# Performance work log

Measured on AMD Instinct MI355X. Metric: run time of the kernel, lower is better.

The kernel has to match this reference:

```python
import jax, jax.numpy as jnp
import numpy as np

N_NODES = 100000
N_EDGES = 1600000
D_IN = 64
D_OUT = 64


def setup_inputs() -> dict:
    key = jax.random.key(0)
    k1, k2, k3, k4, k5 = jax.random.split(key, 5)
    features = jax.random.normal(k1, (N_NODES, D_IN), dtype=jnp.float32)
    edge_row = jax.random.randint(k2, (N_EDGES,), 0, N_NODES, dtype=jnp.int32)
    edge_col = jax.random.randint(k3, (N_EDGES,), 0, N_NODES, dtype=jnp.int32)
    edge_val = jax.random.uniform(k4, (N_EDGES,), dtype=jnp.float32)
    # learned parameters (xavier-uniform kernel, zero bias, ones skip weight)
    limit = float(np.sqrt(6.0 / (D_IN + D_OUT)))
    kernel = jax.random.uniform(k5, (D_IN, D_OUT), minval=-limit, maxval=limit, dtype=jnp.float32)
    bias = jnp.zeros((D_OUT,), dtype=jnp.float32)
    skip_weight = jnp.ones((D_OUT,), dtype=jnp.float32)
    return {
        "features": features,
        "kernel": kernel,
        "bias": bias,
        "skip_weight": skip_weight,
        "edge_row": edge_row,
        "edge_col": edge_col,
        "edge_val": edge_val,
    }


def reference(features, kernel, bias, skip_weight, edge_row, edge_col, edge_val):
    # dense projection: [n, d_in] @ [d_in, d_out]
    h = features @ kernel
    # SpMM: (A h)[r] = sum_{edges e with row r} val_e * h[col_e]
    gathered = h[edge_col] * edge_val[:, None]  # [n_edges, d_out]
    agg = jax.ops.segment_sum(gathered, edge_row, num_segments=N_NODES)
    out = h * skip_weight + agg + bias
    return jax.nn.selu(out)
```

## Files before the change

kernel.cpp:

```cpp
#include <hip/hip_runtime.h>
#include <math.h>

#define N_NODES 100000
#define N_EDGES 1600000
#define D 64
#define RPB 128
#define NBUK 782
#define CAP 3072
#define NGB 782
#define NHB 196
#define EPB 8192
#define POFF_STRIDE 200

typedef unsigned int u32;
typedef unsigned short u16;

static __device__ __forceinline__ u32 f2bf(float x) {
    u32 u = __float_as_uint(x);
    u32 r = u + 0x7FFFu + ((u >> 16) & 1u);
    return r >> 16;
}
static __device__ __forceinline__ u32 pack2(float a, float b) {
    return f2bf(a) | (f2bf(b) << 16);
}
static __device__ __forceinline__ float bflo(u32 u) { return __uint_as_float(u << 16); }
static __device__ __forceinline__ float bfhi(u32 u) { return __uint_as_float(u & 0xFFFF0000u); }
static __device__ __forceinline__ float selu(float x) {
    const float scale = 1.0507009873554805f;
    const float alpha = 1.6732632423543772f;
    return x > 0.f ? scale * x : scale * alpha * (expf(x) - 1.f);
}

__global__ __launch_bounds__(256) void fused_gemm_sort(
    const float* __restrict__ feat, const float* __restrict__ kern,
    const int* __restrict__ erow, const int* __restrict__ ecol,
    const float* __restrict__ eval, u16* __restrict__ hbf,
    int2* __restrict__ sedge, u32* __restrict__ poff)
{
    __shared__ u32 smem[10795];
    const int t = threadIdx.x;

    if (blockIdx.x < NGB) {
        float* ks = (float*)smem;
        {
            const float4* k4 = (const float4*)kern;
            float4* ks4 = (float4*)ks;
            #pragma unroll
            for (int i = 0; i < 4; i++) ks4[t + 256 * i] = k4[t + 256 * i];
        }
        __syncthreads();

        const int cgi  = t & 7;
        const int rg   = t >> 3;
        const int row0 = blockIdx.x * RPB + rg * 4;

        float4 acc[4][2];
        #pragma unroll
        for (int r = 0; r < 4; r++)
            #pragma unroll
            for (int i = 0; i < 2; i++)
                acc[r][i] = make_float4(0.f, 0.f, 0.f, 0.f);

        #pragma unroll 4
        for (int s = 0; s < 16; s++) {
            float4 f[4];
            #pragma unroll
            for (int r = 0; r < 4; r++) {
                int row = min(row0 + r, N_NODES - 1);
                f[r] = ((const float4*)(feat + (size_t)row * D))[s];
            }
            float4 kk[4][2];
            #pragma unroll
            for (int kv = 0; kv < 4; kv++)
                #pragma unroll
                for (int i = 0; i < 2; i++)
                    kk[kv][i] = ((const float4*)(ks + (s * 4 + kv) * D))[cgi * 2 + i];
            #pragma unroll
            for (int r = 0; r < 4; r++) {
                #pragma unroll
                for (int kv = 0; kv < 4; kv++) {
                    float fv = (&f[r].x)[kv];
                    #pragma unroll
                    for (int i = 0; i < 2; i++) {
                        acc[r][i].x += fv * kk[kv][i].x;
                        acc[r][i].y += fv * kk[kv][i].y;
                        acc[r][i].z += fv * kk[kv][i].z;
                        acc[r][i].w += fv * kk[kv][i].w;
                    }
                }
            }
        }

        #pragma unroll
        for (int r = 0; r < 4; r++) {
            int row = row0 + r;
            if (row < N_NODES) {
                uint4 o;
                o.x = pack2(acc[r][0].x, acc[r][0].y);
                o.y = pack2(acc[r][0].z, acc[r][0].w);
                o.z = pack2(acc[r][1].x, acc[r][1].y);
                o.w = pack2(acc[r][1].z, acc[r][1].w);
                ((uint4*)(hbf + (size_t)row * D))[cgi] = o;
            }
        }
    } else {
        u32* er   = smem;
        u32* c    = smem + 8192;
        u32* o    = c + NBUK;
        u32* cu   = o + NBUK + 1;
        u32* part = cu + NBUK;

        for (int i = t; i < NBUK; i += 256) c[i] = 0u;
        __syncthreads();

        const int hb   = blockIdx.x - NGB;
        const int base = hb * EPB;

        #pragma unroll
        for (int k = 0; k < 32; k++) {
            int i = base + k * 256 + t;
            u32 r = 0xFFFFFFFFu;
            if (i < N_EDGES) { r = (u32)erow[i]; atomicAdd(&c[r >> 7], 1u); }
            er[k * 256 + t] = r;
        }
        __syncthreads();

        const int i0 = t * 4;
        {
            u32 p = 0u;
            #pragma unroll
            for (int j = 0; j < 4; j++) { int i = i0 + j; if (i < NBUK) p += c[i]; }
            part[t] = p;
        }
        __syncthreads();
        for (int d = 1; d < 256; d <<= 1) {
            u32 a = (t >= d) ? part[t - d] : 0u;
            __syncthreads();
            part[t] += a;
            __syncthreads();
        }
        {
            u32 run = (t > 0) ? part[t - 1] : 0u;
            #pragma unroll
            for (int j = 0; j < 4; j++) {
                int i = i0 + j;
                if (i < NBUK) { o[i] = run; cu[i] = run; run += c[i]; }
            }
            if (t == 255) o[NBUK] = part[255];
        }
        __syncthreads();

        #pragma unroll
        for (int k = 0; k < 32; k++) {
            int i = base + k * 256 + t;
            if (i < N_EDGES) {
                u32 r = er[k * 256 + t];
                u32 rk = atomicAdd(&cu[r >> 7], 1u);
                sedge[(size_t)hb * EPB + rk] =
                    make_int2(ecol[i] | (int)((r & 127u) << 17),
                              __float_as_int(eval[i]));
            }
        }

        for (int i = t; i <= NBUK; i += 256)
            poff[(size_t)i * POFF_STRIDE + hb] = o[i];
    }
}

__global__ __launch_bounds__(1024) void agg_kernel(
    const u32* __restrict__ poff, const int2* __restrict__ sedge,
    const u16* __restrict__ hbf, const float* __restrict__ skip,
    const float* __restrict__ bias, float* __restrict__ out)
{
    __shared__ int2 eB[CAP];
    __shared__ u32 c[RPB];
    __shared__ u32 o[RPB];
    __shared__ u32 cur[RPB];
    __shared__ u32 rs0[NHB];
    __shared__ u32 rlen[NHB];

    const int t = threadIdx.x;
    const int w = t >> 6;
    const int lane = t & 63;
    const int b = blockIdx.x;

    if (t < RPB) c[t] = 0u;
    if (t < NHB) {
        u32 s0 = poff[(size_t)b * POFF_STRIDE + t];
        u32 s1 = poff[(size_t)(b + 1) * POFF_STRIDE + t];
        rs0[t]  = s0;
        rlen[t] = s1 - s0;
    }
    __syncthreads();

    for (int hb = w; hb < NHB; hb += 16) {
        u32 s0 = rs0[hb], len = rlen[hb];
        for (u32 j = (u32)lane; j < len; j += 64u) {
            int x = sedge[(size_t)hb * EPB + s0 + j].x;
            atomicAdd(&c[(u32)x >> 17], 1u);
        }
    }
    __syncthreads();

    if (t < RPB) o[t] = c[t];
    __syncthreads();
    for (int d = 1; d < RPB; d <<= 1) {
        u32 a = 0u;
        if (t < RPB && t >= d) a = o[t - d];
        __syncthreads();
        if (t < RPB) o[t] += a;
        __syncthreads();
    }
    if (t < RPB) { u32 e = o[t] - c[t]; o[t] = e; cur[t] = e; }
    __syncthreads();

    for (int hb = w; hb < NHB; hb += 16) {
        u32 s0 = rs0[hb], len = rlen[hb];
        for (u32 j = (u32)lane; j < len; j += 64u) {
            int2 e = sedge[(size_t)hb * EPB + s0 + j];
            u32 rl = (u32)e.x >> 17;
            u32 rk = atomicAdd(&cur[rl], 1u);
            if (rk < CAP) eB[rk] = make_int2(e.x & 0x1FFFF, e.y);
        }
    }
    __syncthreads();

    const int rows = min(RPB, N_NODES - b * RPB);
    const int g  = t >> 3;
    const int dg = t & 7;

    float a0 = 0.f, a1 = 0.f, a2 = 0.f, a3 = 0.f;
    float a4 = 0.f, a5 = 0.f, a6 = 0.f, a7 = 0.f;

    u32 jb = 0u, jend = 0u;
    if (g < rows) {
        jb = o[g];
        jend = min(jb + c[g], (u32)CAP);
    }

    u32 j = jb;
    for (; j + 1u < jend; j += 2u) {
        int2 e0 = eB[j];
        int2 e1 = eB[j + 1u];
        float v0 = __int_as_float(e0.y);
        float v1 = __int_as_float(e1.y);
        uint4 h0 = ((const uint4*)(hbf + (size_t)e0.x * D))[dg];
        uint4 h1 = ((const uint4*)(hbf + (size_t)e1.x * D))[dg];
        a0 += v0 * bflo(h0.x); a1 += v0 * bfhi(h0.x);
        a2 += v0 * bflo(h0.y); a3 += v0 * bfhi(h0.y);
        a4 += v0 * bflo(h0.z); a5 += v0 * bfhi(h0.z);
        a6 += v0 * bflo(h0.w); a7 += v0 * bfhi(h0.w);
        a0 += v1 * bflo(h1.x); a1 += v1 * bfhi(h1.x);
        a2 += v1 * bflo(h1.y); a3 += v1 * bfhi(h1.y);
        a4 += v1 * bflo(h1.z); a5 += v1 * bfhi(h1.z);
        a6 += v1 * bflo(h1.w); a7 += v1 * bfhi(h1.w);
    }
    if (j < jend) {
        int2 e0 = eB[j];
        float v0 = __int_as_float(e0.y);
        uint4 h0 = ((const uint4*)(hbf + (size_t)e0.x * D))[dg];
        a0 += v0 * bflo(h0.x); a1 += v0 * bfhi(h0.x);
        a2 += v0 * bflo(h0.y); a3 += v0 * bfhi(h0.y);
        a4 += v0 * bflo(h0.z); a5 += v0 * bfhi(h0.z);
        a6 += v0 * bflo(h0.w); a7 += v0 * bfhi(h0.w);
    }

    if (g < rows) {
        const int grow = b * RPB + g;
        uint4 hr = ((const uint4*)(hbf + (size_t)grow * D))[dg];
        float4 s0 = ((const float4*)skip)[2 * dg];
        float4 s1 = ((const float4*)skip)[2 * dg + 1];
        float4 b0 = ((const float4*)bias)[2 * dg];
        float4 b1 = ((const float4*)bias)[2 * dg + 1];
        float4 x0, x1;
        x0.x = selu(bflo(hr.x) * s0.x + b0.x + a0);
        x0.y = selu(bfhi(hr.x) * s0.y + b0.y + a1);
        x0.z = selu(bflo(hr.y) * s0.z + b0.z + a2);
        x0.w = selu(bfhi(hr.y) * s0.w + b0.w + a3);
        x1.x = selu(bflo(hr.z) * s1.x + b1.x + a4);
        x1.y = selu(bfhi(hr.z) * s1.y + b1.y + a5);
        x1.z = selu(bflo(hr.w) * s1.z + b1.z + a6);
        x1.w = selu(bfhi(hr.w) * s1.w + b1.w + a7);
        ((float4*)(out + (size_t)grow * D))[2 * dg]     = x0;
        ((float4*)(out + (size_t)grow * D))[2 * dg + 1] = x1;
    }
}

extern "C" void kernel_launch(void* const* d_in, const int* in_sizes, int n_in,
                              void* d_out, int out_size, void* d_ws, size_t ws_size,
                              hipStream_t stream)
{
    const float* feat = (const float*)d_in[0];
    const float* kern = (const float*)d_in[1];
    const float* bias = (const float*)d_in[2];
    const float* skip = (const float*)d_in[3];
    const int*   erow = (const int*)d_in[4];
    const int*   ecol = (const int*)d_in[5];
    const float* eval = (const float*)d_in[6];
    float* out = (float*)d_out;

    u16*  hbf   = (u16*)d_ws;
    u32*  poff  = (u32*)(hbf + (size_t)N_NODES * D);
    int2* sedge = (int2*)(poff + 156600);

    hipLaunchKernelGGL(fused_gemm_sort, dim3(NGB + NHB), dim3(256), 0, stream,
                       feat, kern, erow, ecol, eval, hbf, sedge, poff);
    hipLaunchKernelGGL(agg_kernel, dim3(NBUK), dim3(1024), 0, stream,
                       poff, sedge, hbf, skip, bias, out);
}
```

Baseline: 183.0 us.

## Split edge bucketing into more smaller blocks, schedule them first, unroll gather by four

The edge histogram/scatter phase now uses 392 blocks of 4096 edges instead of 196 blocks of 8192, and these blocks are placed first in the grid so sorting starts earlier alongside the GEMM blocks. The per-block row cache in shared memory is dropped and erow is re-read from global memory, which cuts LDS use from about 43KB to 16KB to allow higher occupancy. The aggregation loop is unrolled to four edges per iteration to keep more gathers in flight. The cost is more partition offsets for the aggregation kernel to read and a second global read of erow.

```diff
diff --git a/kernel.cpp b/kernel.cpp
--- a/kernel.cpp
+++ b/kernel.cpp
@@ -8,9 +8,9 @@
 #define NBUK 782
 #define CAP 3072
 #define NGB 782
-#define NHB 196
-#define EPB 8192
-#define POFF_STRIDE 200
+#define NHB 392
+#define EPB 4096
+#define POFF_STRIDE 392
 
 typedef unsigned int u32;
 typedef unsigned short u16;
@@ -37,10 +37,10 @@
     const float* __restrict__ eval, u16* __restrict__ hbf,
     int2* __restrict__ sedge, u32* __restrict__ poff)
 {
-    __shared__ u32 smem[10795];
+    __shared__ u32 smem[4096];
     const int t = threadIdx.x;
 
-    if (blockIdx.x < NGB) {
+    if (blockIdx.x >= NHB) {
         float* ks = (float*)smem;
         {
             const float4* k4 = (const float4*)kern;
@@ -52,7 +52,7 @@
 
         const int cgi  = t & 7;
         const int rg   = t >> 3;
-        const int row0 = blockIdx.x * RPB + rg * 4;
+        const int row0 = (blockIdx.x - NHB) * RPB + rg * 4;
 
         float4 acc[4][2];
         #pragma unroll
@@ -104,8 +104,7 @@
             }
         }
     } else {
-        u32* er   = smem;
-        u32* c    = smem + 8192;
+        u32* c    = smem;
         u32* o    = c + NBUK;
         u32* cu   = o + NBUK + 1;
         u32* part = cu + NBUK;
@@ -113,15 +112,13 @@
         for (int i = t; i < NBUK; i += 256) c[i] = 0u;
         __syncthreads();
 
-        const int hb   = blockIdx.x - NGB;
+        const int hb   = blockIdx.x;
         const int base = hb * EPB;
 
         #pragma unroll
-        for (int k = 0; k < 32; k++) {
+        for (int k = 0; k < 16; k++) {
             int i = base + k * 256 + t;
-            u32 r = 0xFFFFFFFFu;
-            if (i < N_EDGES) { r = (u32)erow[i]; atomicAdd(&c[r >> 7], 1u); }
-            er[k * 256 + t] = r;
+            if (i < N_EDGES) atomicAdd(&c[(u32)erow[i] >> 7], 1u);
         }
         __syncthreads();
 
@@ -151,10 +148,10 @@
         __syncthreads();
 
         #pragma unroll
-        for (int k = 0; k < 32; k++) {
+        for (int k = 0; k < 16; k++) {
             int i = base + k * 256 + t;
             if (i < N_EDGES) {
-                u32 r = er[k * 256 + t];
+                u32 r = (u32)erow[i];
                 u32 rk = atomicAdd(&cu[r >> 7], 1u);
                 sedge[(size_t)hb * EPB + rk] =
                     make_int2(ecol[i] | (int)((r & 127u) << 17),
@@ -239,13 +236,19 @@
     }
 
     u32 j = jb;
-    for (; j + 1u < jend; j += 2u) {
+    for (; j + 3u < jend; j += 4u) {
         int2 e0 = eB[j];
         int2 e1 = eB[j + 1u];
+        int2 e2 = eB[j + 2u];
+        int2 e3 = eB[j + 3u];
         float v0 = __int_as_float(e0.y);
         float v1 = __int_as_float(e1.y);
+        float v2 = __int_as_float(e2.y);
+        float v3 = __int_as_float(e3.y);
         uint4 h0 = ((const uint4*)(hbf + (size_t)e0.x * D))[dg];
         uint4 h1 = ((const uint4*)(hbf + (size_t)e1.x * D))[dg];
+        uint4 h2 = ((const uint4*)(hbf + (size_t)e2.x * D))[dg];
+        uint4 h3 = ((const uint4*)(hbf + (size_t)e3.x * D))[dg];
         a0 += v0 * bflo(h0.x); a1 += v0 * bfhi(h0.x);
         a2 += v0 * bflo(h0.y); a3 += v0 * bfhi(h0.y);
         a4 += v0 * bflo(h0.z); a5 += v0 * bfhi(h0.z);
@@ -254,8 +257,16 @@
         a2 += v1 * bflo(h1.y); a3 += v1 * bfhi(h1.y);
         a4 += v1 * bflo(h1.z); a5 += v1 * bfhi(h1.z);
         a6 += v1 * bflo(h1.w); a7 += v1 * bfhi(h1.w);
-    }
-    if (j < jend) {
+        a0 += v2 * bflo(h2.x); a1 += v2 * bfhi(h2.x);
+        a2 += v2 * bflo(h2.y); a3 += v2 * bfhi(h2.y);
+        a4 += v2 * bflo(h2.z); a5 += v2 * bfhi(h2.z);
+        a6 += v2 * bflo(h2.w); a7 += v2 * bfhi(h2.w);
+        a0 += v3 * bflo(h3.x); a1 += v3 * bfhi(h3.x);
+        a2 += v3 * bflo(h3.y); a3 += v3 * bfhi(h3.y);
+        a4 += v3 * bflo(h3.z); a5 += v3 * bfhi(h3.z);
+        a6 += v3 * bflo(h3.w); a7 += v3 * bfhi(h3.w);
+    }
+    for (; j < jend; j++) {
         int2 e0 = eB[j];
         float v0 = __int_as_float(e0.y);
         uint4 h0 = ((const uint4*)(hbf + (size_t)e0.x * D))[dg];
@@ -301,7 +312,7 @@
 
     u16*  hbf   = (u16*)d_ws;
     u32*  poff  = (u32*)(hbf + (size_t)N_NODES * D);
-    int2* sedge = (int2*)(poff + 156600);
+    int2* sedge = (int2*)(poff + 306936);
 
     hipLaunchKernelGGL(fused_gemm_sort, dim3(NGB + NHB), dim3(256), 0, stream,
                        feat, kern, erow, ecol, eval, hbf, sedge, poff);
```

After: 195.0 us. 1.07x slower.
